# Kernel optimization log

Measured on AMD Instinct MI355X. Metric: run time of the kernel, lower is better.

The kernel has to match this reference:

```python
import jax, jax.numpy as jnp
import numpy as np

B, N_ATOM, COORD = 32, 48, 3
N_ELEM = 4
GRID_SIZE = 128
SIGMA = 0.05      # gaussian broadening of distf
W_SCALE = 1.0     # weightf: exp(-W_SCALE * distance)
INV_SQRT2PI = 1.0 / np.sqrt(2.0 * np.pi)


def _pairs(n):
    # static ordered index pairs i != j (built with numpy -> jit-safe constants)
    ii, jj = np.meshgrid(np.arange(n), np.arange(n), indexing='ij')
    m = ii != jj
    return jnp.asarray(ii[m]), jnp.asarray(jj[m])


def setup_inputs() -> dict:
    key = jax.random.key(0)
    k1, k2 = jax.random.split(key)
    r = jax.random.normal(k1, (B, N_ATOM, COORD), dtype=jnp.float32) * 2.0
    z = jax.random.randint(k2, (N_ATOM,), 0, N_ELEM)  # species index in [0, N_ELEM)
    grid = jnp.linspace(0.0, 2.0, GRID_SIZE, dtype=jnp.float32)
    return {"r": r, "z": z, "grid": grid}


def reference(r, z, grid):
    b, n, c = r.shape
    g = grid.shape[0]
    e = N_ELEM
    dx = grid[1] - grid[0]
    pi, pj = _pairs(n)                              # (P,)

    diff = r[:, pi] - r[:, pj]                      # (b,P,3)
    d = jnp.sqrt(jnp.sum(diff * diff, axis=-1))     # (b,P) pair distances
    gf = 1.0 / d                                    # geomf: inverse distance
    wf = jnp.exp(-W_SCALE * d)                      # weightf: exponential decay
    # distf: normalized gaussian centered at gf, scaled by grid spacing dx
    t = (grid[None, None, :] - gf[..., None]) / SIGMA
    gv = jnp.exp(-0.5 * t * t) * (dx * INV_SQRT2PI / SIGMA)   # (b,P,G)

    contrib = wf[..., None] * gv                    # (b,P,G)
    seg = z[pi] * e + z[pj]                         # (P,) element-pair bucket
    mbtr = jax.ops.segment_sum(contrib.transpose(1, 0, 2), seg, num_segments=e * e)
    mbtr = mbtr.reshape(e, e, b, g).transpose(2, 0, 1, 3)      # (b,E,E,G)

    # analytic divergence wrt the two atoms' coordinates (order=2, coord=3)
    u = diff / d[..., None]                         # dd/dr_i, (b,P,3)
    dd = jnp.stack([u, -u], axis=2)                 # (b,P,2,3): dd/dr_{i}, dd/dr_{j}
    gf_div = -(gf * gf)[..., None, None] * dd       # d(1/d)/dr
    wf_div = -(W_SCALE * wf)[..., None, None] * dd  # d exp(-s d)/dr
    grid_div = gv * (grid[None, None, :] - gf[..., None]) / (SIGMA * SIGMA)  # dgv/dgf

    # (b,P,G,2,3): gv*wf_div + grid_div*gf_div*wf
    div = (gv[:, :, :, None, None] * wf_div[:, :, None, :, :]
           + grid_div[:, :, :, None, None] * (gf_div * wf[..., None, None])[:, :, None, :, :])

    atom_idx = jnp.stack([pi, pj], axis=1)          # (P,2)
    seg_div = (seg[:, None] * n + atom_idx).reshape(-1)        # (2P,) bucket*n + atom
    p2 = div.transpose(1, 3, 0, 2, 4).reshape(-1, b, g, c)     # (2P,b,G,3)
    mbtr_div = jax.ops.segment_sum(p2, seg_div, num_segments=e * e * n)
    mbtr_div = mbtr_div.reshape(e, e, n, b, g, c).transpose(3, 0, 1, 4, 2, 5)  # (b,E,E,G,N,3)
    return mbtr, mbtr_div
```

## Files before the change

### kernel.cpp

```cpp
#include <hip/hip_runtime.h>

#define NB     32
#define NATOM  48
#define NGRID  128
#define KT     8
#define NTHR   384

#define MBTR_ELEMS (NB*16*NGRID)
#define DIV_PER_B  (16*NGRID*NATOM*3)
#define PANE       (NGRID*NATOM*3)
#define MSTRIDE    49

__global__ __launch_bounds__(NTHR)
void mbtr_fused(const float* __restrict__ r, const int* __restrict__ z,
                const float* __restrict__ grid, float* __restrict__ out)
{
    const int kt = blockIdx.x, b = blockIdx.y, t = threadIdx.x;
    const int k0 = kt * KT;

    __shared__ float4 pos[NATOM];
    __shared__ int    zl[NATOM];
    __shared__ int    order[NATOM];
    __shared__ int    soff_s[5];
    __shared__ float  Mrec[KT * 4 * MSTRIDE];

    if (t < 64) {
        const bool isatom = (t < NATOM);
        int myz = 999;
        if (isatom) {
            myz = z[t];
            zl[t] = myz;
            const float* rp = r + ((size_t)b * NATOM + t) * 3;
            pos[t] = make_float4(rp[0], rp[1], rp[2], 0.f);
        }
        const unsigned long long m0 = __ballot(myz == 0);
        const unsigned long long m1 = __ballot(myz == 1);
        const unsigned long long m2 = __ballot(myz == 2);
        const unsigned long long m3 = __ballot(myz == 3);
        const int c0 = __popcll(m0), c1 = __popcll(m1), c2 = __popcll(m2);
        if (isatom) {
            const unsigned long long mm = (myz == 0) ? m0 : (myz == 1) ? m1
                                        : (myz == 2) ? m2 : m3;
            const int base = (myz == 0) ? 0 : (myz == 1) ? c0
                           : (myz == 2) ? c0 + c1 : c0 + c1 + c2;
            const int rank = __popcll(mm & ((1ull << t) - 1ull));
            order[base + rank] = t;
        }
        if (t == 0) {
            soff_s[0] = 0; soff_s[1] = c0; soff_s[2] = c0 + c1;
            soff_s[3] = c0 + c1 + c2; soff_s[4] = NATOM;
        }
    }
    __syncthreads();

    const int n  = t % NATOM;
    const int kk = t / NATOM;
    const float dx   = grid[1] - grid[0];
    const float coef = dx * 7.9788456080286535f;
    const float mlc  = -__log2f(coef);
    const float isc  = 16.986436005760382f;
    const float tBc  = 23.548200452219559f;
    const float l2e  = 1.4426950408889634f;
    const float gk   = grid[k0 + kk] * isc;

    float A[4][3] = {{0.f}};
    float M[4]    = {0.f};
    const float4 rn = pos[n];
    const int   zn  = zl[n];
    int so[5];
    #pragma unroll
    for (int e = 0; e < 5; ++e) so[e] = soff_s[e];

    #pragma unroll
    for (int e = 0; e < 4; ++e) {
        for (int i = so[e]; i < so[e + 1]; ++i) {
            const int    m  = order[i];
            const float4 rm = pos[m];
            const float ddx = rn.x - rm.x, ddy = rn.y - rm.y, ddz = rn.z - rm.z;
            float d2 = ddx*ddx + ddy*ddy + ddz*ddz;
            const bool self = (m == n);
            d2 = self ? 1.0f : d2;
            const float gf  = __builtin_amdgcn_rsqf(d2);
            const float c1  = gf * isc;
            const float d   = d2 * gf;
            float base = fmaf(d, l2e, mlc);
            base = self ? 1e30f : base;
            const float bq  = (gf * gf) * tBc;
            const float tt  = gk - c1;
            const float ex  = exp2f(-fmaf(tt, tt, base));
            M[e] += ex;
            const float p   = ex * fmaf(tt, bq, 1.0f);
            A[e][0] = fmaf(-p, gf * ddx, A[e][0]);
            A[e][1] = fmaf(-p, gf * ddy, A[e][1]);
            A[e][2] = fmaf(-p, gf * ddz, A[e][2]);
        }
    }

    {
        float* mr = Mrec + kk * (4 * MSTRIDE) + n;
        #pragma unroll
        for (int e = 0; e < 4; ++e) mr[e * MSTRIDE] = M[e];
    }

    float* basep = out + MBTR_ELEMS + (size_t)b * DIV_PER_B
                 + (size_t)(k0 + kk) * 144 + n * 3;
    #pragma unroll
    for (int e1 = 0; e1 < 4; ++e1) {
        const bool s1 = (zn == e1);
        #pragma unroll
        for (int e2 = 0; e2 < 4; ++e2) {
            const bool s2 = (zn == e2);
            float* p = basep + (e1 * 4 + e2) * PANE;
            p[0] = (s1 ? A[e2][0] : 0.f) + (s2 ? A[e1][0] : 0.f);
            p[1] = (s1 ? A[e2][1] : 0.f) + (s2 ? A[e1][1] : 0.f);
            p[2] = (s1 ? A[e2][2] : 0.f) + (s2 ? A[e1][2] : 0.f);
        }
    }

    __syncthreads();

    if (t < 128) {
        const int mpane = t >> 3, mkk = t & 7;
        const int me1 = mpane >> 2, me2 = mpane & 3;
        const float* tr2 = Mrec + mkk * (4 * MSTRIDE) + me2 * MSTRIDE;
        float s = 0.f;
        #pragma unroll
        for (int nn = 0; nn < NATOM; ++nn)
            s += (zl[nn] == me1) ? tr2[nn] : 0.f;
        out[(size_t)b * 2048 + mpane * NGRID + k0 + mkk] = s;
    }
}

extern "C" void kernel_launch(void* const* d_in, const int* in_sizes, int n_in,
                              void* d_out, int out_size, void* d_ws, size_t ws_size,
                              hipStream_t stream)
{
    const float* r    = (const float*)d_in[0];
    const int*   z    = (const int*)  d_in[1];
    const float* grid = (const float*)d_in[2];
    float* out = (float*)d_out;
    (void)d_ws; (void)ws_size;

    mbtr_fused<<<dim3(NGRID / KT, NB), NTHR, 0, stream>>>(r, z, grid, out);
}
```

Before: 80.75 us.

## Compute two grid points per thread to reuse pair geometry across grid tiles

```diff
diff --git a/kernel.cpp b/kernel.cpp
--- a/kernel.cpp
+++ b/kernel.cpp
@@ -3,7 +3,7 @@
 #define NB     32
 #define NATOM  48
 #define NGRID  128
-#define KT     8
+#define KT     16
 #define NTHR   384
 
 #define MBTR_ELEMS (NB*16*NGRID)
@@ -54,17 +54,18 @@
     __syncthreads();
 
     const int n  = t % NATOM;
-    const int kk = t / NATOM;
+    const int kq = t / NATOM;
     const float dx   = grid[1] - grid[0];
     const float coef = dx * 7.9788456080286535f;
     const float mlc  = -__log2f(coef);
     const float isc  = 16.986436005760382f;
     const float tBc  = 23.548200452219559f;
     const float l2e  = 1.4426950408889634f;
-    const float gk   = grid[k0 + kk] * isc;
+    const float gkA  = grid[k0 + kq]     * isc;
+    const float gkB  = grid[k0 + kq + 8] * isc;
 
-    float A[4][3] = {{0.f}};
-    float M[4]    = {0.f};
+    float A[2][4][3] = {{{0.f}}};
+    float M[2][4]    = {{0.f}};
     const float4 rn = pos[n];
     const int   zn  = zl[n];
     int so[5];
@@ -86,41 +87,41 @@
             float base = fmaf(d, l2e, mlc);
             base = self ? 1e30f : base;
             const float bq  = (gf * gf) * tBc;
-            const float tt  = gk - c1;
-            const float ex  = exp2f(-fmaf(tt, tt, base));
-            M[e] += ex;
-            const float p   = ex * fmaf(tt, bq, 1.0f);
-            A[e][0] = fmaf(-p, gf * ddx, A[e][0]);
-            A[e][1] = fmaf(-p, gf * ddy, A[e][1]);
-            A[e][2] = fmaf(-p, gf * ddz, A[e][2]);
+            const float sux = gf * ddx, suy = gf * ddy, suz = gf * ddz;
+            {
+                const float tt = gkA - c1;
+                const float ex = exp2f(-fmaf(tt, tt, base));
+                M[0][e] += ex;
+                const float p  = ex * fmaf(tt, bq, 1.0f);
+                A[0][e][0] = fmaf(-p, sux, A[0][e][0]);
+                A[0][e][1] = fmaf(-p, suy, A[0][e][1]);
+                A[0][e][2] = fmaf(-p, suz, A[0][e][2]);
+            }
+            {
+                const float tt = gkB - c1;
+                const float ex = exp2f(-fmaf(tt, tt, base));
+                M[1][e] += ex;
+                const float p  = ex * fmaf(tt, bq, 1.0f);
+                A[1][e][0] = fmaf(-p, sux, A[1][e][0]);
+                A[1][e][1] = fmaf(-p, suy, A[1][e][1]);
+                A[1][e][2] = fmaf(-p, suz, A[1][e][2]);
+            }
         }
     }
 
     {
-        float* mr = Mrec + kk * (4 * MSTRIDE) + n;
+        float* mr0 = Mrec + kq       * (4 * MSTRIDE) + n;
+        float* mr1 = Mrec + (kq + 8) * (4 * MSTRIDE) + n;
         #pragma unroll
-        for (int e = 0; e < 4; ++e) mr[e * MSTRIDE] = M[e];
-    }
-
-    float* basep = out + MBTR_ELEMS + (size_t)b * DIV_PER_B
-                 + (size_t)(k0 + kk) * 144 + n * 3;
-    #pragma unroll
-    for (int e1 = 0; e1 < 4; ++e1) {
-        const bool s1 = (zn == e1);
-        #pragma unroll
-        for (int e2 = 0; e2 < 4; ++e2) {
-            const bool s2 = (zn == e2);
-            float* p = basep + (e1 * 4 + e2) * PANE;
-            p[0] = (s1 ? A[e2][0] : 0.f) + (s2 ? A[e1][0] : 0.f);
-            p[1] = (s1 ? A[e2][1] : 0.f) + (s2 ? A[e1][1] : 0.f);
-            p[2] = (s1 ? A[e2][2] : 0.f) + (s2 ? A[e1][2] : 0.f);
+        for (int e = 0; e < 4; ++e) {
+            mr0[e * MSTRIDE] = M[0][e];
+            mr1[e * MSTRIDE] = M[1][e];
         }
     }
-
     __syncthreads();
 
-    if (t < 128) {
-        const int mpane = t >> 3, mkk = t & 7;
+    if (t < 256) {
+        const int mpane = t >> 4, mkk = t & 15;
         const int me1 = mpane >> 2, me2 = mpane & 3;
         const float* tr2 = Mrec + mkk * (4 * MSTRIDE) + me2 * MSTRIDE;
         float s = 0.f;
@@ -128,6 +129,25 @@
         for (int nn = 0; nn < NATOM; ++nn)
             s += (zl[nn] == me1) ? tr2[nn] : 0.f;
         out[(size_t)b * 2048 + mpane * NGRID + k0 + mkk] = s;
+    }
+
+    float* divout = out + MBTR_ELEMS + (size_t)b * DIV_PER_B;
+    #pragma unroll
+    for (int h = 0; h < 2; ++h) {
+        float* basep = divout + (size_t)(k0 + kq + 8 * h) * 144 + n * 3;
+        #pragma unroll
+        for (int e1 = 0; e1 < 4; ++e1) {
+            const bool s1 = (zn == e1);
+            #pragma unroll
+            for (int e2 = 0; e2 < 4; ++e2) {
+                const bool s2 = (zn == e2);
+                float3 v;
+                v.x = (s1 ? A[h][e2][0] : 0.f) + (s2 ? A[h][e1][0] : 0.f);
+                v.y = (s1 ? A[h][e2][1] : 0.f) + (s2 ? A[h][e1][1] : 0.f);
+                v.z = (s1 ? A[h][e2][2] : 0.f) + (s2 ? A[h][e1][2] : 0.f);
+                *(float3*)(basep + (e1 * 4 + e2) * PANE) = v;
+            }
+        }
     }
 }
 
```

Result: no change. 80.77 us (+0.0%).
